# Kernel tuning notes

Hardware: AMD Instinct MI355X
Metric: run time of the kernel (lower is better)

## Reference

```python
import jax, jax.numpy as jnp
import numpy as np

H = 256


def _lstm_cell(inp, hx, cx, Wih, Whh, bih, bhh):
    # PyTorch LSTMCell: gate order i, f, g, o
    gates = inp @ Wih.T + bih + hx @ Whh.T + bhh
    i, f, g, o = jnp.split(gates, 4, axis=-1)
    c = jax.nn.sigmoid(f) * cx + jax.nn.sigmoid(i) * jnp.tanh(g)
    h = jax.nn.sigmoid(o) * jnp.tanh(c)
    return h, c


def _match(p_enc, q_enc, wq, wp, whr_w, whr_b, w_vec, w_b0, Wih, Whh, bih, bhh, reverse):
    # p_enc: (P,B,H) time-major passage; q_enc, wq: (Q,B,H); wp: (P,B,H)
    B = p_enc.shape[1]

    def step(carry, xs):
        hx, cx = carry
        wphp, p_t = xs                                  # (B,H), (B,H)
        wrhr = hx @ whr_w.T + whr_b                     # (B,H)
        g = jnp.tanh(wq + (wphp + wrhr))                # (Q,B,H)
        scores = jnp.einsum('qbh,h->bq', g, w_vec) + w_b0
        alpha = jax.nn.softmax(scores, axis=-1)         # (B,Q)
        attn = jnp.einsum('bq,qbh->bh', alpha, q_enc)   # (B,H)
        inp = jnp.concatenate([p_t, attn], axis=-1)     # (B,2H)
        hx, cx = _lstm_cell(inp, hx, cx, Wih, Whh, bih, bhh)
        return (hx, cx), hx

    init = (jnp.zeros((B, H), p_enc.dtype), jnp.zeros((B, H), p_enc.dtype))
    _, hs = jax.lax.scan(step, init, (wp, p_enc), reverse=reverse)
    return hs  # (P,B,H), always in natural time order


def setup_inputs() -> dict:
    key = jax.random.key(0)
    ks = jax.random.split(key, 20)
    s = 0.05
    return {
        'passage': jax.random.normal(ks[0], (64, 512, H), jnp.float32),
        'question': jax.random.normal(ks[1], (64, 64, H), jnp.float32),
        'whq_w': jax.random.normal(ks[2], (H, H), jnp.float32) * s,
        'whq_b': jax.random.normal(ks[3], (H,), jnp.float32) * s,
        'whp_w': jax.random.normal(ks[4], (H, H), jnp.float32) * s,
        'whp_b': jax.random.normal(ks[5], (H,), jnp.float32) * s,
        'whr_w': jax.random.normal(ks[6], (H, H), jnp.float32) * s,
        'whr_b': jax.random.normal(ks[7], (H,), jnp.float32) * s,
        'w_w': jax.random.normal(ks[8], (1, H), jnp.float32) * s,
        'w_b': jax.random.normal(ks[9], (1,), jnp.float32) * s,
        'fw_Wih': jax.random.normal(ks[10], (4 * H, 2 * H), jnp.float32) * s,
        'fw_Whh': jax.random.normal(ks[11], (4 * H, H), jnp.float32) * s,
        'fw_bih': jax.random.normal(ks[12], (4 * H,), jnp.float32) * s,
        'fw_bhh': jax.random.normal(ks[13], (4 * H,), jnp.float32) * s,
        'bw_Wih': jax.random.normal(ks[14], (4 * H, 2 * H), jnp.float32) * s,
        'bw_Whh': jax.random.normal(ks[15], (4 * H, H), jnp.float32) * s,
        'bw_bih': jax.random.normal(ks[16], (4 * H,), jnp.float32) * s,
        'bw_bhh': jax.random.normal(ks[17], (4 * H,), jnp.float32) * s,
    }


def reference(passage, question, whq_w, whq_b, whp_w, whp_b, whr_w, whr_b,
              w_w, w_b, fw_Wih, fw_Whh, fw_bih, fw_bhh,
              bw_Wih, bw_Whh, bw_bih, bw_bhh):
    p = jnp.swapaxes(passage, 0, 1)    # (P,B,H)
    q = jnp.swapaxes(question, 0, 1)   # (Q,B,H)
    wq = q @ whq_w.T + whq_b           # (Q,B,H)  (dropout p=0.0 -> identity)
    wp = p @ whp_w.T + whp_b           # (P,B,H)
    fw = _match(p, q, wq, wp, whr_w, whr_b, w_w[0], w_b[0],
                fw_Wih, fw_Whh, fw_bih, fw_bhh, reverse=False)
    bw = _match(p, q, wq, wp, whr_w, whr_b, w_w[0], w_b[0],
                bw_Wih, bw_Whh, bw_bih, bw_bhh, reverse=True)
    return jnp.concatenate([fw, bw], axis=-1)  # (P,B,2H)
```

## Files before the change

### kernel.cpp

```cpp
#include <hip/hip_runtime.h>

#define HN 256
#define QN 64
#define PN 512
#define CH 8

typedef float f4 __attribute__((ext_vector_type(4)));

__device__ __forceinline__ float dot4(f4 a, f4 b) {
  return a.x * b.x + a.y * b.y + a.z * b.z + a.w * b.w;
}
__device__ __forceinline__ float fast_sig(float x) {
  return __builtin_amdgcn_rcpf(1.f + __builtin_amdgcn_exp2f(-1.44269504f * x));
}
__device__ __forceinline__ float fast_tanh(float x) {
  return 1.f - 2.f * __builtin_amdgcn_rcpf(1.f + __builtin_amdgcn_exp2f(2.88539008f * x));
}
__device__ __forceinline__ float red16(float v) {
  v += __shfl_xor(v, 1); v += __shfl_xor(v, 2);
  v += __shfl_xor(v, 4); v += __shfl_xor(v, 8);
  return v;
}
__device__ __forceinline__ f4 red16v(f4 v) {
  v.x = red16(v.x); v.y = red16(v.y); v.z = red16(v.z); v.w = red16(v.w);
  return v;
}

struct SMem {
  union {
    float q32[QN][HN];
    struct {
      alignas(16) float pgc[CH][1024];
      alignas(16) float wpc[CH][HN];
      alignas(16) float pch[CH][HN];
    } c;
  } u;
  alignas(16) float wqt[QN][HN + 4];
  alignas(16) float ww[HN];
  alignas(16) float hx[HN];
  float cx[HN];
  alignas(16) float wA[HN];
  float wrb[HN];
  float gates[1024];
  float scores[QN];
  alignas(16) float al[QN];
};
static_assert(sizeof(SMem) <= 160 * 1024, "LDS overflow");
static_assert(sizeof(SMem) > 80 * 1024, "want exactly 1 block/CU");

__global__ void
__attribute__((amdgpu_flat_work_group_size(1024, 1024)))
__attribute__((amdgpu_waves_per_eu(1, 4)))
match_kernel(const float* __restrict__ passage, const float* __restrict__ question,
             const float* __restrict__ whq_w, const float* __restrict__ whq_b,
             const float* __restrict__ whp_w, const float* __restrict__ whp_b,
             const float* __restrict__ whr_w, const float* __restrict__ whr_b,
             const float* __restrict__ w_w,
             const float* __restrict__ Wih_f, const float* __restrict__ Whh_f,
             const float* __restrict__ bih_f, const float* __restrict__ bhh_f,
             const float* __restrict__ Wih_b, const float* __restrict__ Whh_b,
             const float* __restrict__ bih_b, const float* __restrict__ bhh_b,
             float* __restrict__ out)
{
  __shared__ SMem sm;
  const int t = threadIdx.x;
  const int bid = blockIdx.x;
  const int e = bid & 7;
  const int dir = e >> 2;
  const int b = ((bid >> 3) << 2) | (e & 3);

  const float* Wih = dir ? Wih_b : Wih_f;
  const float* Whh = dir ? Whh_b : Whh_f;
  const float* bih = dir ? bih_b : bih_f;
  const float* bhh = dir ? bhh_b : bhh_f;

  const int qB = t >> 4;
  const int sg = t & 15;
  const int g2 = t >> 4;

  {
    const int q = t >> 4, c0 = (t & 15) * 16;
    const float* src = question + ((size_t)b * QN + q) * HN + c0;
    #pragma unroll
    for (int m = 0; m < 4; ++m)
      *(f4*)&sm.u.q32[q][c0 + 4 * m] = *(const f4*)(src + 4 * m);
  }
  if (t < HN) {
    sm.hx[t] = 0.f; sm.cx[t] = 0.f;
    sm.wrb[t] = whr_b[t]; sm.ww[t] = w_w[t];
  }
  __syncthreads();

  {
    const int h = t & 255, qh = (t >> 8) * 16;
    const float qb = whq_b[h];
    f4 ac0, ac1, ac2, ac3;
    ac0.x = ac0.y = ac0.z = ac0.w = qb;
    ac1 = ac0; ac2 = ac0; ac3 = ac0;
    const float* wrow = whq_w + (size_t)h * HN;
    for (int k = 0; k < HN; k += 4) {
      f4 w4 = *(const f4*)(wrow + k);
      #define WQ4(V, Q0) \
        V.x += dot4(w4, *(const f4*)&sm.u.q32[qh + (Q0) + 0][k]); \
        V.y += dot4(w4, *(const f4*)&sm.u.q32[qh + (Q0) + 1][k]); \
        V.z += dot4(w4, *(const f4*)&sm.u.q32[qh + (Q0) + 2][k]); \
        V.w += dot4(w4, *(const f4*)&sm.u.q32[qh + (Q0) + 3][k]);
      WQ4(ac0, 0) WQ4(ac1, 4) WQ4(ac2, 8) WQ4(ac3, 12)
      #undef WQ4
    }
    sm.wqt[qh + 0][h] = ac0.x;  sm.wqt[qh + 1][h] = ac0.y;
    sm.wqt[qh + 2][h] = ac0.z;  sm.wqt[qh + 3][h] = ac0.w;
    sm.wqt[qh + 4][h] = ac1.x;  sm.wqt[qh + 5][h] = ac1.y;
    sm.wqt[qh + 6][h] = ac1.z;  sm.wqt[qh + 7][h] = ac1.w;
    sm.wqt[qh + 8][h] = ac2.x;  sm.wqt[qh + 9][h] = ac2.y;
    sm.wqt[qh + 10][h] = ac2.z; sm.wqt[qh + 11][h] = ac2.w;
    sm.wqt[qh + 12][h] = ac3.x; sm.wqt[qh + 13][h] = ac3.y;
    sm.wqt[qh + 14][h] = ac3.z; sm.wqt[qh + 15][h] = ac3.w;
  }

  f4 gq00 = {0.f, 0.f, 0.f, 0.f};
  f4 gq01 = gq00, gq02 = gq00, gq03 = gq00, gq04 = gq00, gq05 = gq00,
     gq06 = gq00, gq07 = gq00, gq08 = gq00, gq09 = gq00, gq10 = gq00,
     gq11 = gq00, gq12 = gq00, gq13 = gq00, gq14 = gq00, gq15 = gq00;
  {
    const float* wrow = Wih + (size_t)t * 512 + 256;
    for (int i = 0; i < 64; ++i) {
      f4 w = *(const f4*)(wrow + 4 * i);
      #define GQ4(V, Q0) \
        V.x += dot4(w, *(const f4*)&sm.u.q32[(Q0) + 0][4 * i]); \
        V.y += dot4(w, *(const f4*)&sm.u.q32[(Q0) + 1][4 * i]); \
        V.z += dot4(w, *(const f4*)&sm.u.q32[(Q0) + 2][4 * i]); \
        V.w += dot4(w, *(const f4*)&sm.u.q32[(Q0) + 3][4 * i]);
      GQ4(gq00, 0)  GQ4(gq01, 4)  GQ4(gq02, 8)  GQ4(gq03, 12)
      GQ4(gq04, 16) GQ4(gq05, 20) GQ4(gq06, 24) GQ4(gq07, 28)
      GQ4(gq08, 32) GQ4(gq09, 36) GQ4(gq10, 40) GQ4(gq11, 44)
      GQ4(gq12, 48) GQ4(gq13, 52) GQ4(gq14, 56) GQ4(gq15, 60)
      #undef GQ4
    }
  }
  const float biasr = bih[t] + bhh[t];
  __syncthreads();

  const int tb = dir ? (PN - 1) : 0;
  const int ts = dir ? -1 : 1;

  for (int s = 0; s < PN; ++s) {
    const int tau = s & (CH - 1);
    if (tau == 0) {
      if (t < 512) {
        const int tt = t >> 6, cc = (t & 63) * 4;
        const int trow = tb + ts * (s + tt);
        *(f4*)&sm.u.c.pch[tt][cc] =
            *(const f4*)(passage + ((size_t)b * PN + trow) * HN + cc);
      }
      __syncthreads();
      #pragma unroll
      for (int rr = 0; rr < 4; ++rr) {
        const int h = g2 + 64 * rr;
        const float* wrow = whp_w + (size_t)h * HN + sg * 4;
        f4 wa0 = {0.f, 0.f, 0.f, 0.f}, wa1 = wa0;
        #pragma unroll
        for (int m = 0; m < 4; ++m) {
          f4 w = *(const f4*)(wrow + m * 64);
          wa0.x += dot4(w, *(const f4*)&sm.u.c.pch[0][m * 64 + sg * 4]);
          wa0.y += dot4(w, *(const f4*)&sm.u.c.pch[1][m * 64 + sg * 4]);
          wa0.z += dot4(w, *(const f4*)&sm.u.c.pch[2][m * 64 + sg * 4]);
          wa0.w += dot4(w, *(const f4*)&sm.u.c.pch[3][m * 64 + sg * 4]);
          wa1.x += dot4(w, *(const f4*)&sm.u.c.pch[4][m * 64 + sg * 4]);
          wa1.y += dot4(w, *(const f4*)&sm.u.c.pch[5][m * 64 + sg * 4]);
          wa1.z += dot4(w, *(const f4*)&sm.u.c.pch[6][m * 64 + sg * 4]);
          wa1.w += dot4(w, *(const f4*)&sm.u.c.pch[7][m * 64 + sg * 4]);
        }
        wa0 = red16v(wa0); wa1 = red16v(wa1);
        if (sg == rr) {
          const float pb = whp_b[h];
          sm.u.c.wpc[0][h] = wa0.x + pb; sm.u.c.wpc[1][h] = wa0.y + pb;
          sm.u.c.wpc[2][h] = wa0.z + pb; sm.u.c.wpc[3][h] = wa0.w + pb;
          sm.u.c.wpc[4][h] = wa1.x + pb; sm.u.c.wpc[5][h] = wa1.y + pb;
          sm.u.c.wpc[6][h] = wa1.z + pb; sm.u.c.wpc[7][h] = wa1.w + pb;
        }
      }
      #pragma unroll
      for (int rr = 0; rr < 16; ++rr) {
        const int r = g2 + 64 * rr;
        const float* wrow = Wih + (size_t)r * 512 + sg * 4;
        f4 pa0 = {0.f, 0.f, 0.f, 0.f}, pa1 = pa0;
        #pragma unroll
        for (int m = 0; m < 4; ++m) {
          f4 w = *(const f4*)(wrow + m * 64);
          pa0.x += dot4(w, *(const f4*)&sm.u.c.pch[0][m * 64 + sg * 4]);
          pa0.y += dot4(w, *(const f4*)&sm.u.c.pch[1][m * 64 + sg * 4]);
          pa0.z += dot4(w, *(const f4*)&sm.u.c.pch[2][m * 64 + sg * 4]);
          pa0.w += dot4(w, *(const f4*)&sm.u.c.pch[3][m * 64 + sg * 4]);
          pa1.x += dot4(w, *(const f4*)&sm.u.c.pch[4][m * 64 + sg * 4]);
          pa1.y += dot4(w, *(const f4*)&sm.u.c.pch[5][m * 64 + sg * 4]);
          pa1.z += dot4(w, *(const f4*)&sm.u.c.pch[6][m * 64 + sg * 4]);
          pa1.w += dot4(w, *(const f4*)&sm.u.c.pch[7][m * 64 + sg * 4]);
        }
        pa0 = red16v(pa0); pa1 = red16v(pa1);
        if (sg == rr) {
          sm.u.c.pgc[0][r] = pa0.x; sm.u.c.pgc[1][r] = pa0.y;
          sm.u.c.pgc[2][r] = pa0.z; sm.u.c.pgc[3][r] = pa0.w;
          sm.u.c.pgc[4][r] = pa1.x; sm.u.c.pgc[5][r] = pa1.y;
          sm.u.c.pgc[6][r] = pa1.z; sm.u.c.pgc[7][r] = pa1.w;
        }
      }
      __syncthreads();
    }

    #pragma unroll
    for (int rr = 0; rr < 4; ++rr) {
      const int h = g2 + 64 * rr;
      const float* wrow = whr_w + (size_t)h * HN + sg * 4;
      float a = 0.f;
      #pragma unroll
      for (int m = 0; m < 4; ++m)
        a += dot4(*(const f4*)(wrow + m * 64),
                  *(const f4*)&sm.hx[m * 64 + sg * 4]);
      a = red16(a);
      if (sg == rr) sm.wA[h] = a + sm.u.c.wpc[tau][h] + sm.wrb[h];
    }
    __syncthreads();

    {
      float sc = 0.f;
      #pragma unroll
      for (int jj = 0; jj < 4; ++jj) {
        f4 a4 = *(const f4*)&sm.wA[sg * 16 + 4 * jj];
        f4 q4 = *(const f4*)&sm.wqt[qB][sg * 16 + 4 * jj];
        f4 w4 = *(const f4*)&sm.ww[sg * 16 + 4 * jj];
        sc += fast_tanh(q4.x + a4.x) * w4.x;
        sc += fast_tanh(q4.y + a4.y) * w4.y;
        sc += fast_tanh(q4.z + a4.z) * w4.z;
        sc += fast_tanh(q4.w + a4.w) * w4.w;
      }
      sc = red16(sc);
      if (sg == 0) sm.scores[qB] = sc;
    }
    __syncthreads();

    #pragma unroll
    for (int rr = 0; rr < 16; ++rr) {
      const int r = g2 + 64 * rr;
      const float* wrow = Whh + (size_t)r * HN + sg * 4;
      float a = 0.f;
      #pragma unroll
      for (int m = 0; m < 4; ++m)
        a += dot4(*(const f4*)(wrow + m * 64),
                  *(const f4*)&sm.hx[m * 64 + sg * 4]);
      a = red16(a);
      if (sg == rr) sm.gates[r] = a;
    }
    if (t < 64) {
      float sv = sm.scores[t];
      float mx = sv;
      #pragma unroll
      for (int o = 1; o < 64; o <<= 1) mx = fmaxf(mx, __shfl_xor(mx, o));
      float ex = __builtin_amdgcn_exp2f(1.44269504f * (sv - mx));
      float sum = ex;
      #pragma unroll
      for (int o = 1; o < 64; o <<= 1) sum += __shfl_xor(sum, o);
      sm.al[t] = ex * __builtin_amdgcn_rcpf(sum);
    }
    __syncthreads();

    {
      float acc = sm.gates[t] + sm.u.c.pgc[tau][t] + biasr;
      acc += dot4(gq00, *(const f4*)&sm.al[0]);
      acc += dot4(gq01, *(const f4*)&sm.al[4]);
      acc += dot4(gq02, *(const f4*)&sm.al[8]);
      acc += dot4(gq03, *(const f4*)&sm.al[12]);
      acc += dot4(gq04, *(const f4*)&sm.al[16]);
      acc += dot4(gq05, *(const f4*)&sm.al[20]);
      acc += dot4(gq06, *(const f4*)&sm.al[24]);
      acc += dot4(gq07, *(const f4*)&sm.al[28]);
      acc += dot4(gq08, *(const f4*)&sm.al[32]);
      acc += dot4(gq09, *(const f4*)&sm.al[36]);
      acc += dot4(gq10, *(const f4*)&sm.al[40]);
      acc += dot4(gq11, *(const f4*)&sm.al[44]);
      acc += dot4(gq12, *(const f4*)&sm.al[48]);
      acc += dot4(gq13, *(const f4*)&sm.al[52]);
      acc += dot4(gq14, *(const f4*)&sm.al[56]);
      acc += dot4(gq15, *(const f4*)&sm.al[60]);
      sm.gates[t] = acc;
    }
    __syncthreads();

    if (t < HN) {
      float gi = sm.gates[t], gf = sm.gates[HN + t];
      float gg = sm.gates[2 * HN + t], go = sm.gates[3 * HN + t];
      float c = fast_sig(gf) * sm.cx[t] + fast_sig(gi) * fast_tanh(gg);
      float hn = fast_sig(go) * fast_tanh(c);
      sm.cx[t] = c;
      sm.hx[t] = hn;
      const int trow = tb + ts * s;
      out[((size_t)trow * 64 + b) * 512 + dir * HN + t] = hn;
    }
    __syncthreads();
  }
}

extern "C" void kernel_launch(void* const* d_in, const int* in_sizes, int n_in,
                              void* d_out, int out_size, void* d_ws, size_t ws_size,
                              hipStream_t stream) {
  (void)in_sizes; (void)n_in; (void)out_size; (void)d_ws; (void)ws_size;
  match_kernel<<<dim3(128), dim3(1024), 0, stream>>>(
      (const float*)d_in[0],
      (const float*)d_in[1],
      (const float*)d_in[2],
      (const float*)d_in[3],
      (const float*)d_in[4],
      (const float*)d_in[5],
      (const float*)d_in[6],
      (const float*)d_in[7],
      (const float*)d_in[8],
      (const float*)d_in[10],
      (const float*)d_in[11],
      (const float*)d_in[12],
      (const float*)d_in[13],
      (const float*)d_in[14],
      (const float*)d_in[15],
      (const float*)d_in[16],
      (const float*)d_in[17],
      (float*)d_out);
}
```

Baseline: 27.18 ms.

## Compute attention vector explicitly and stream Wih attn half per step

Replaces the precomputed per-thread Wih·q projections (64 register-held gate contributions combined with alpha each step) with an explicit attention vector (alpha·q) followed by a per-step Wih[:,256:] matvec streamed from global/cache. The LSTM bias is folded into the chunked passage-gate precompute, and the wq row and w_w slice are hoisted into registers for the score loop. This frees the 64 f4 registers and the long prologue, but adds a 256x1024 matvec read per timestep plus an extra barrier.

Result: slower. 67.30 ms (median of 2 runs) (+147.7%).

```diff
diff --git a/kernel.cpp b/kernel.cpp
--- a/kernel.cpp
+++ b/kernel.cpp
@@ -27,20 +27,20 @@
 }
 
 struct SMem {
+  alignas(16) float q32[QN][HN];
   union {
-    float q32[QN][HN];
+    float wqt[QN][HN + 4];
     struct {
       alignas(16) float pgc[CH][1024];
       alignas(16) float wpc[CH][HN];
       alignas(16) float pch[CH][HN];
     } c;
   } u;
-  alignas(16) float wqt[QN][HN + 4];
-  alignas(16) float ww[HN];
   alignas(16) float hx[HN];
   float cx[HN];
   alignas(16) float wA[HN];
   float wrb[HN];
+  alignas(16) float attn[HN];
   float gates[1024];
   float scores[QN];
   alignas(16) float al[QN];
@@ -48,9 +48,7 @@
 static_assert(sizeof(SMem) <= 160 * 1024, "LDS overflow");
 static_assert(sizeof(SMem) > 80 * 1024, "want exactly 1 block/CU");
 
-__global__ void
-__attribute__((amdgpu_flat_work_group_size(1024, 1024)))
-__attribute__((amdgpu_waves_per_eu(1, 4)))
+__global__ void __launch_bounds__(1024)
 match_kernel(const float* __restrict__ passage, const float* __restrict__ question,
              const float* __restrict__ whq_w, const float* __restrict__ whq_b,
              const float* __restrict__ whp_w, const float* __restrict__ whp_b,
@@ -83,11 +81,11 @@
     const float* src = question + ((size_t)b * QN + q) * HN + c0;
     #pragma unroll
     for (int m = 0; m < 4; ++m)
-      *(f4*)&sm.u.q32[q][c0 + 4 * m] = *(const f4*)(src + 4 * m);
+      *(f4*)&sm.q32[q][c0 + 4 * m] = *(const f4*)(src + 4 * m);
   }
   if (t < HN) {
     sm.hx[t] = 0.f; sm.cx[t] = 0.f;
-    sm.wrb[t] = whr_b[t]; sm.ww[t] = w_w[t];
+    sm.wrb[t] = whr_b[t];
   }
   __syncthreads();
 
@@ -101,44 +99,34 @@
     for (int k = 0; k < HN; k += 4) {
       f4 w4 = *(const f4*)(wrow + k);
       #define WQ4(V, Q0) \
-        V.x += dot4(w4, *(const f4*)&sm.u.q32[qh + (Q0) + 0][k]); \
-        V.y += dot4(w4, *(const f4*)&sm.u.q32[qh + (Q0) + 1][k]); \
-        V.z += dot4(w4, *(const f4*)&sm.u.q32[qh + (Q0) + 2][k]); \
-        V.w += dot4(w4, *(const f4*)&sm.u.q32[qh + (Q0) + 3][k]);
+        V.x += dot4(w4, *(const f4*)&sm.q32[qh + (Q0) + 0][k]); \
+        V.y += dot4(w4, *(const f4*)&sm.q32[qh + (Q0) + 1][k]); \
+        V.z += dot4(w4, *(const f4*)&sm.q32[qh + (Q0) + 2][k]); \
+        V.w += dot4(w4, *(const f4*)&sm.q32[qh + (Q0) + 3][k]);
       WQ4(ac0, 0) WQ4(ac1, 4) WQ4(ac2, 8) WQ4(ac3, 12)
       #undef WQ4
     }
-    sm.wqt[qh + 0][h] = ac0.x;  sm.wqt[qh + 1][h] = ac0.y;
-    sm.wqt[qh + 2][h] = ac0.z;  sm.wqt[qh + 3][h] = ac0.w;
-    sm.wqt[qh + 4][h] = ac1.x;  sm.wqt[qh + 5][h] = ac1.y;
-    sm.wqt[qh + 6][h] = ac1.z;  sm.wqt[qh + 7][h] = ac1.w;
-    sm.wqt[qh + 8][h] = ac2.x;  sm.wqt[qh + 9][h] = ac2.y;
-    sm.wqt[qh + 10][h] = ac2.z; sm.wqt[qh + 11][h] = ac2.w;
-    sm.wqt[qh + 12][h] = ac3.x; sm.wqt[qh + 13][h] = ac3.y;
-    sm.wqt[qh + 14][h] = ac3.z; sm.wqt[qh + 15][h] = ac3.w;
+    sm.u.wqt[qh + 0][h] = ac0.x;  sm.u.wqt[qh + 1][h] = ac0.y;
+    sm.u.wqt[qh + 2][h] = ac0.z;  sm.u.wqt[qh + 3][h] = ac0.w;
+    sm.u.wqt[qh + 4][h] = ac1.x;  sm.u.wqt[qh + 5][h] = ac1.y;
+    sm.u.wqt[qh + 6][h] = ac1.z;  sm.u.wqt[qh + 7][h] = ac1.w;
+    sm.u.wqt[qh + 8][h] = ac2.x;  sm.u.wqt[qh + 9][h] = ac2.y;
+    sm.u.wqt[qh + 10][h] = ac2.z; sm.u.wqt[qh + 11][h] = ac2.w;
+    sm.u.wqt[qh + 12][h] = ac3.x; sm.u.wqt[qh + 13][h] = ac3.y;
+    sm.u.wqt[qh + 14][h] = ac3.z; sm.u.wqt[qh + 15][h] = ac3.w;
   }
-
-  f4 gq00 = {0.f, 0.f, 0.f, 0.f};
-  f4 gq01 = gq00, gq02 = gq00, gq03 = gq00, gq04 = gq00, gq05 = gq00,
-     gq06 = gq00, gq07 = gq00, gq08 = gq00, gq09 = gq00, gq10 = gq00,
-     gq11 = gq00, gq12 = gq00, gq13 = gq00, gq14 = gq00, gq15 = gq00;
-  {
-    const float* wrow = Wih + (size_t)t * 512 + 256;
-    for (int i = 0; i < 64; ++i) {
-      f4 w = *(const f4*)(wrow + 4 * i);
-      #define GQ4(V, Q0) \
-        V.x += dot4(w, *(const f4*)&sm.u.q32[(Q0) + 0][4 * i]); \
-        V.y += dot4(w, *(const f4*)&sm.u.q32[(Q0) + 1][4 * i]); \
-        V.z += dot4(w, *(const f4*)&sm.u.q32[(Q0) + 2][4 * i]); \
-        V.w += dot4(w, *(const f4*)&sm.u.q32[(Q0) + 3][4 * i]);
-      GQ4(gq00, 0)  GQ4(gq01, 4)  GQ4(gq02, 8)  GQ4(gq03, 12)
-      GQ4(gq04, 16) GQ4(gq05, 20) GQ4(gq06, 24) GQ4(gq07, 28)
-      GQ4(gq08, 32) GQ4(gq09, 36) GQ4(gq10, 40) GQ4(gq11, 44)
-      GQ4(gq12, 48) GQ4(gq13, 52) GQ4(gq14, 56) GQ4(gq15, 60)
-      #undef GQ4
-    }
-  }
-  const float biasr = bih[t] + bhh[t];
+  __syncthreads();
+
+  f4 wq0 = *(const f4*)&sm.u.wqt[qB][sg * 16 + 0];
+  f4 wq1 = *(const f4*)&sm.u.wqt[qB][sg * 16 + 4];
+  f4 wq2 = *(const f4*)&sm.u.wqt[qB][sg * 16 + 8];
+  f4 wq3 = *(const f4*)&sm.u.wqt[qB][sg * 16 + 12];
+  f4 ww0 = *(const f4*)(w_w + sg * 16 + 0);
+  f4 ww1 = *(const f4*)(w_w + sg * 16 + 4);
+  f4 ww2 = *(const f4*)(w_w + sg * 16 + 8);
+  f4 ww3 = *(const f4*)(w_w + sg * 16 + 12);
+  const int rE = g2 + 64 * sg;
+  const float biasE = bih[rE] + bhh[rE];
   __syncthreads();
 
   const int tb = dir ? (PN - 1) : 0;
@@ -199,10 +187,10 @@
         }
         pa0 = red16v(pa0); pa1 = red16v(pa1);
         if (sg == rr) {
-          sm.u.c.pgc[0][r] = pa0.x; sm.u.c.pgc[1][r] = pa0.y;
-          sm.u.c.pgc[2][r] = pa0.z; sm.u.c.pgc[3][r] = pa0.w;
-          sm.u.c.pgc[4][r] = pa1.x; sm.u.c.pgc[5][r] = pa1.y;
-          sm.u.c.pgc[6][r] = pa1.z; sm.u.c.pgc[7][r] = pa1.w;
+          sm.u.c.pgc[0][r] = pa0.x + biasE; sm.u.c.pgc[1][r] = pa0.y + biasE;
+          sm.u.c.pgc[2][r] = pa0.z + biasE; sm.u.c.pgc[3][r] = pa0.w + biasE;
+          sm.u.c.pgc[4][r] = pa1.x + biasE; sm.u.c.pgc[5][r] = pa1.y + biasE;
+          sm.u.c.pgc[6][r] = pa1.z + biasE; sm.u.c.pgc[7][r] = pa1.w + biasE;
         }
       }
       __syncthreads();
@@ -223,17 +211,27 @@
     __syncthreads();
 
     {
+      f4 a0 = *(const f4*)&sm.wA[sg * 16 + 0];
+      f4 a1 = *(const f4*)&sm.wA[sg * 16 + 4];
+      f4 a2 = *(const f4*)&sm.wA[sg * 16 + 8];
+      f4 a3 = *(const f4*)&sm.wA[sg * 16 + 12];
       float sc = 0.f;
-      #pragma unroll
-      for (int jj = 0; jj < 4; ++jj) {
-        f4 a4 = *(const f4*)&sm.wA[sg * 16 + 4 * jj];
-        f4 q4 = *(const f4*)&sm.wqt[qB][sg * 16 + 4 * jj];
-        f4 w4 = *(const f4*)&sm.ww[sg * 16 + 4 * jj];
-        sc += fast_tanh(q4.x + a4.x) * w4.x;
-        sc += fast_tanh(q4.y + a4.y) * w4.y;
-        sc += fast_tanh(q4.z + a4.z) * w4.z;
-        sc += fast_tanh(q4.w + a4.w) * w4.w;
-      }
+      sc += fast_tanh(wq0.x + a0.x) * ww0.x;
+      sc += fast_tanh(wq0.y + a0.y) * ww0.y;
+      sc += fast_tanh(wq0.z + a0.z) * ww0.z;
+      sc += fast_tanh(wq0.w + a0.w) * ww0.w;
+      sc += fast_tanh(wq1.x + a1.x) * ww1.x;
+      sc += fast_tanh(wq1.y + a1.y) * ww1.y;
+      sc += fast_tanh(wq1.z + a1.z) * ww1.z;
+      sc += fast_tanh(wq1.w + a1.w) * ww1.w;
+      sc += fast_tanh(wq2.x + a2.x) * ww2.x;
+      sc += fast_tanh(wq2.y + a2.y) * ww2.y;
+      sc += fast_tanh(wq2.z + a2.z) * ww2.z;
+      sc += fast_tanh(wq2.w + a2.w) * ww2.w;
+      sc += fast_tanh(wq3.x + a3.x) * ww3.x;
+      sc += fast_tanh(wq3.y + a3.y) * ww3.y;
+      sc += fast_tanh(wq3.z + a3.z) * ww3.z;
+      sc += fast_tanh(wq3.w + a3.w) * ww3.w;
       sc = red16(sc);
       if (sg == 0) sm.scores[qB] = sc;
     }
@@ -264,25 +262,26 @@
     }
     __syncthreads();
 
-    {
-      float acc = sm.gates[t] + sm.u.c.pgc[tau][t] + biasr;
-      acc += dot4(gq00, *(const f4*)&sm.al[0]);
-      acc += dot4(gq01, *(const f4*)&sm.al[4]);
-      acc += dot4(gq02, *(const f4*)&sm.al[8]);
-      acc += dot4(gq03, *(const f4*)&sm.al[12]);
-      acc += dot4(gq04, *(const f4*)&sm.al[16]);
-      acc += dot4(gq05, *(const f4*)&sm.al[20]);
-      acc += dot4(gq06, *(const f4*)&sm.al[24]);
-      acc += dot4(gq07, *(const f4*)&sm.al[28]);
-      acc += dot4(gq08, *(const f4*)&sm.al[32]);
-      acc += dot4(gq09, *(const f4*)&sm.al[36]);
-      acc += dot4(gq10, *(const f4*)&sm.al[40]);
-      acc += dot4(gq11, *(const f4*)&sm.al[44]);
-      acc += dot4(gq12, *(const f4*)&sm.al[48]);
-      acc += dot4(gq13, *(const f4*)&sm.al[52]);
-      acc += dot4(gq14, *(const f4*)&sm.al[56]);
-      acc += dot4(gq15, *(const f4*)&sm.al[60]);
-      sm.gates[t] = acc;
+    if (t < HN) {
+      float a = 0.f;
+      #pragma unroll 16
+      for (int q = 0; q < QN; ++q)
+        a += sm.al[q] * sm.q32[q][t];
+      sm.attn[t] = a;
+    }
+    __syncthreads();
+
+    #pragma unroll
+    for (int rr = 0; rr < 16; ++rr) {
+      const int r = g2 + 64 * rr;
+      const float* wrow = Wih + (size_t)r * 512 + 256 + sg * 4;
+      float a = 0.f;
+      #pragma unroll
+      for (int m = 0; m < 4; ++m)
+        a += dot4(*(const f4*)(wrow + m * 64),
+                  *(const f4*)&sm.attn[m * 64 + sg * 4]);
+      a = red16(a);
+      if (sg == rr) sm.gates[r] += a + sm.u.c.pgc[tau][r];
     }
     __syncthreads();
 
```
